# Kernel tuning notes

Hardware: AMD Instinct MI355X
Metric: run time of the kernel (lower is better)

## Reference

```python
import jax, jax.numpy as jnp
import numpy as np

TIME_UNITS = 10.0
EPS_LN = 1e-5
N_NODES, N_EDGES, BATCH, T_IN = 20000, 320000, 8, 12
H_PROB, H_VEL = 64, 32


def _layernorm(x, g, b):
    mu = jnp.mean(x, axis=-1, keepdims=True)
    var = jnp.mean((x - mu) ** 2, axis=-1, keepdims=True)
    return (x - mu) / jnp.sqrt(var + EPS_LN) * g + b


def setup_inputs() -> dict:
    key = jax.random.key(0)
    ks = jax.random.split(key, 20)
    s = 0.1
    inp = {}
    inp['upstream'] = jax.random.uniform(ks[0], (N_EDGES, BATCH, T_IN), jnp.float32)
    inp['downstream'] = jax.random.uniform(ks[1], (N_EDGES, BATCH, T_IN), jnp.float32)
    inp['feature'] = jax.random.uniform(ks[2], (N_NODES, BATCH, T_IN), jnp.float32)
    inp['distance'] = jax.random.uniform(ks[3], (N_EDGES,), jnp.float32, 10.0, 500.0)
    inp['src'] = jax.random.randint(ks[4], (N_EDGES,), 0, N_NODES, jnp.int32)
    inp['dst'] = jax.random.randint(ks[5], (N_EDGES,), 0, N_NODES, jnp.int32)
    inp['fc_w'] = jax.random.normal(ks[6], (H_PROB, T_IN), jnp.float32) * s
    inp['attn_w'] = jax.random.normal(ks[7], (1, 2 * H_PROB + 1), jnp.float32) * s
    inp['ln2_g'] = jnp.ones((2 * H_PROB + 1,), jnp.float32)
    inp['ln2_b'] = jnp.zeros((2 * H_PROB + 1,), jnp.float32)
    inp['v11_w'] = jax.random.normal(ks[8], (H_VEL, T_IN), jnp.float32) * s
    inp['v11_b'] = jnp.zeros((H_VEL,), jnp.float32)
    inp['ln11_g'] = jnp.ones((H_VEL,), jnp.float32)
    inp['ln11_b'] = jnp.zeros((H_VEL,), jnp.float32)
    inp['v12_w'] = jax.random.normal(ks[9], (1, H_VEL), jnp.float32) * s
    inp['v12_b'] = jnp.zeros((1,), jnp.float32)
    inp['v21_w'] = jax.random.normal(ks[10], (H_VEL, T_IN), jnp.float32) * s
    inp['v21_b'] = jnp.zeros((H_VEL,), jnp.float32)
    inp['ln21_g'] = jnp.ones((H_VEL,), jnp.float32)
    inp['ln21_b'] = jnp.zeros((H_VEL,), jnp.float32)
    inp['v22_w'] = jax.random.normal(ks[11], (1, H_VEL), jnp.float32) * s
    inp['v22_b'] = jnp.zeros((1,), jnp.float32)
    inp['v3_w'] = jax.random.normal(ks[12], (1, 2), jnp.float32) * s
    inp['v3_b'] = jnp.zeros((1,), jnp.float32)
    inp['alpha'] = jnp.ones((N_EDGES, 1), jnp.float32)
    return inp


def reference(upstream, downstream, feature, distance, src, dst,
              fc_w, attn_w, ln2_g, ln2_b,
              v11_w, v11_b, ln11_g, ln11_b, v12_w, v12_b,
              v21_w, v21_b, ln21_g, ln21_b, v22_w, v22_b,
              v3_w, v3_b, alpha):
    N, B, T = feature.shape
    Tf = jnp.asarray(T, feature.dtype)

    # --- Velocity_Model_NAM (eval mode: dropout = identity) ---
    def branch(x, w1, b1, g, bn, w2, b2):
        h = jax.nn.relu(_layernorm(x @ w1.T + b1, g, bn))
        return jax.nn.sigmoid(h @ w2.T + b2)  # [E,B,1]

    xu = branch(upstream, v11_w, v11_b, ln11_g, ln11_b, v12_w, v12_b)
    xd = branch(downstream, v21_w, v21_b, ln21_g, ln21_b, v22_w, v22_b)
    v = jnp.log1p(jnp.exp((jnp.concatenate([xu, xd], -1) @ v3_w.T + v3_b)[..., 0]))  # [E,B]

    # --- per-edge travel time and diffusion kernel ---
    Tt = distance[:, None] / (v + 1e-5)                # [E,B]
    T_idx = jnp.round(Tt / TIME_UNITS)
    T_idx = jnp.where(T_idx < 0, 0.0, T_idx)
    T_idx = jnp.where(T_idx > Tf, Tf - 1.0, T_idx)     # strictly > T_in, as in masked_fill
    F = 1.0 / (1.0 + alpha * Tt)                       # [E,B]
    n = jnp.maximum(Tf - T_idx, 1.0)                   # sequence length per (edge,batch)
    t = jnp.arange(T, dtype=feature.dtype)
    mask = t < n[..., None]
    expo = jnp.maximum(n[..., None] - 1.0 - t, 0.0)    # decreasing exponents n-1..0
    diffusion = jnp.where(mask, F[..., None] * jnp.power(1.0 - F[..., None], expo), 0.0)  # [E,B,T]

    # --- Probabilistic_Model: embeddings + edge softmax normalized per SOURCE node ---
    z = feature @ fc_w.T                               # [N,B,64]
    zc = jnp.concatenate([z[src], z[dst], jax.lax.stop_gradient(v)[..., None]], -1)  # [E,B,129]
    a = jax.nn.leaky_relu((_layernorm(zc, ln2_g, ln2_b) @ attn_w.T)[..., 0], 0.01)   # [E,B]
    m = jax.ops.segment_max(a, src, num_segments=N)
    ex = jnp.exp(a - m[src])
    den = jax.ops.segment_sum(ex, src, num_segments=N)
    score = ex / den[src]

    # --- mailbox reduce: attention-weighted diffusion prediction per destination ---
    pred_edge = jnp.sum(diffusion * feature[src], -1)  # [E,B]
    pred = jax.ops.segment_sum(score * pred_edge, dst, num_segments=N)  # [N,B]
    return pred
```

## Files before the change

kernel.cpp:

```cpp
#include <hip/hip_runtime.h>
#include <math.h>

#define TB 8
#define TT 12
#define HV 32

typedef float v2f __attribute__((ext_vector_type(2)));

__device__ __forceinline__ float vel_branch32(const v2f xv[6],
    const float* __restrict__ w1, const float* __restrict__ b1,
    const float* __restrict__ g,  const float* __restrict__ bn,
    const float* __restrict__ w2, float b2) {
  v2f h2[HV/2];
  v2f s1v = {0.f, 0.f}, s2v = {0.f, 0.f};
#pragma unroll
  for (int jp = 0; jp < HV/2; ++jp) {
    const float* w0 = w1 + (2*jp)   * TT;
    const float* w1r = w1 + (2*jp+1) * TT;
    v2f p0 = {0.f, 0.f}, p1 = {0.f, 0.f};
#pragma unroll
    for (int k = 0; k < 6; ++k) {
      p0 = __builtin_elementwise_fma(xv[k], *(const v2f*)(w0  + 2*k), p0);
      p1 = __builtin_elementwise_fma(xv[k], *(const v2f*)(w1r + 2*k), p1);
    }
    v2f bj = *(const v2f*)(b1 + 2*jp);
    v2f hv = {p0.x + p0.y + bj.x, p1.x + p1.y + bj.y};
    h2[jp] = hv;
    s1v += hv;
    s2v = __builtin_elementwise_fma(hv, hv, s2v);
  }
  float s1 = s1v.x + s1v.y;
  float s2 = s2v.x + s2v.y;
  float mu  = s1 * (1.f/HV);
  float var = s2 * (1.f/HV) - mu*mu;
  float inv = 1.f / sqrtf(var + 1e-5f);
  v2f mu2  = {mu, mu};
  v2f inv2 = {inv, inv};
  v2f zero = {0.f, 0.f};
  v2f acc2 = {b2, 0.f};
#pragma unroll
  for (int jp = 0; jp < HV/2; ++jp) {
    v2f gv  = *(const v2f*)(g  + 2*jp);
    v2f bnv = *(const v2f*)(bn + 2*jp);
    v2f w2v = *(const v2f*)(w2 + 2*jp);
    v2f yl = __builtin_elementwise_fma((h2[jp] - mu2) * inv2, gv, bnv);
    yl = __builtin_elementwise_max(yl, zero);
    acc2 = __builtin_elementwise_fma(yl, w2v, acc2);
  }
  float acc = acc2.x + acc2.y;
  return 1.f / (1.f + __expf(-acc));
}

__device__ __noinline__ double vel_branch64(const float* x,
    const float* __restrict__ w1, const float* __restrict__ b1,
    const float* __restrict__ g,  const float* __restrict__ bn,
    const float* __restrict__ w2, float b2) {
  double s1 = 0.0, s2 = 0.0;
  for (int j = 0; j < HV; ++j) {
    double hj = (double)b1[j];
    for (int t = 0; t < TT; ++t) hj = fma((double)x[t], (double)w1[j*TT+t], hj);
    s1 += hj;
    s2 = fma(hj, hj, s2);
  }
  double mu  = s1 / (double)HV;
  double var = s2 / (double)HV - mu*mu;
  double inv = 1.0 / sqrt(var + 1e-5);
  double acc = (double)b2;
  for (int j = 0; j < HV; ++j) {
    double hj = (double)b1[j];
    for (int t = 0; t < TT; ++t) hj = fma((double)x[t], (double)w1[j*TT+t], hj);
    double yl = (hj - mu) * inv * (double)g[j] + (double)bn[j];
    if (yl < 0.0) yl = 0.0;
    acc = fma(yl, (double)w2[j], acc);
  }
  return 1.0 / (1.0 + exp(-acc));
}

__global__ void __launch_bounds__(256) k_zero_prep(
    float* __restrict__ den, float* __restrict__ pred, int nb,
    const float* __restrict__ attn_w, const float* __restrict__ ln2_g,
    const float* __restrict__ ln2_b, float* __restrict__ scal) {
  int idx = blockIdx.x * blockDim.x + threadIdx.x;
  for (int i = idx; i < nb; i += gridDim.x * blockDim.x) { den[i] = 0.f; pred[i] = 0.f; }
  if (blockIdx.x == 0) {
    __shared__ float sg[256], sb[256];
    float a = 0.f, b = 0.f;
    if (threadIdx.x < 129) {
      float w = attn_w[threadIdx.x];
      a = w * ln2_g[threadIdx.x];
      b = w * ln2_b[threadIdx.x];
    }
    sg[threadIdx.x] = a; sb[threadIdx.x] = b;
    __syncthreads();
    for (int s = 128; s > 0; s >>= 1) {
      if (threadIdx.x < s) { sg[threadIdx.x] += sg[threadIdx.x+s]; sb[threadIdx.x] += sb[threadIdx.x+s]; }
      __syncthreads();
    }
    if (threadIdx.x == 0) { scal[0] = sg[0]; scal[1] = sb[0]; }
  }
}

__global__ void __launch_bounds__(256, 2) k_node(
    const float* __restrict__ feature, const float* __restrict__ fc_w,
    const float* __restrict__ attn_w,  const float* __restrict__ ln2_g,
    float4* __restrict__ nodepre, int n_nodes) {
  int idx = blockIdx.x * blockDim.x + threadIdx.x;
  int total = n_nodes * TB;
  if (idx >= total) return;
  const float4* f4 = (const float4*)(feature + (size_t)idx * TT);
  float4 fa = f4[0], fb = f4[1], fcv = f4[2];
  v2f xv[6] = {{fa.x,fa.y},{fa.z,fa.w},{fb.x,fb.y},{fb.z,fb.w},{fcv.x,fcv.y},{fcv.z,fcv.w}};
  float q = 0.f, r = 0.f, ps = 0.f, pd = 0.f;
#pragma unroll 8
  for (int i = 0; i < 64; ++i) {
    v2f p = {0.f, 0.f};
#pragma unroll
    for (int k = 0; k < 6; ++k)
      p = __builtin_elementwise_fma(xv[k], *(const v2f*)(fc_w + i*TT + 2*k), p);
    float z = p.x + p.y;
    q += z;
    r  = fmaf(z, z, r);
    ps = fmaf(z, attn_w[i]      * ln2_g[i],      ps);
    pd = fmaf(z, attn_w[64 + i] * ln2_g[64 + i], pd);
  }
  nodepre[idx] = make_float4(q, r, ps, pd);
}

__global__ void __launch_bounds__(256, 2) k_edge1(
    const float* __restrict__ upstream, const float* __restrict__ downstream,
    const float* __restrict__ feature,  const float* __restrict__ distance,
    const int* __restrict__ src, const int* __restrict__ dst,
    const float* __restrict__ attn_w, const float* __restrict__ ln2_g,
    const float* __restrict__ v11_w, const float* __restrict__ v11_b,
    const float* __restrict__ ln11_g, const float* __restrict__ ln11_b,
    const float* __restrict__ v12_w, const float* __restrict__ v12_b,
    const float* __restrict__ v21_w, const float* __restrict__ v21_b,
    const float* __restrict__ ln21_g, const float* __restrict__ ln21_b,
    const float* __restrict__ v22_w, const float* __restrict__ v22_b,
    const float* __restrict__ v3_w, const float* __restrict__ v3_b,
    const float* __restrict__ alpha,
    const float4* __restrict__ nodepre, const float* __restrict__ scal,
    float2* __restrict__ epbuf, float* __restrict__ den,
    int n_edges) {
  int idx = blockIdx.x * blockDim.x + threadIdx.x;
  if (idx >= n_edges * TB) return;
  int e = idx >> 3, b = idx & 7;

  int s = src[e], d = dst[e];
  float dist = distance[e];
  float al   = alpha[e];
  const float4* f4 = (const float4*)(feature + ((size_t)s * TB + b) * TT);
  float4 f0 = f4[0], f1 = f4[1], f2 = f4[2];
  float4 nps = nodepre[(size_t)s * TB + b];
  float4 npd = nodepre[(size_t)d * TB + b];

  float xu, xd;
  {
    const float4* u4 = (const float4*)(upstream + (size_t)idx * TT);
    float4 a0 = u4[0], a1 = u4[1], a2 = u4[2];
    v2f xv[6] = {{a0.x,a0.y},{a0.z,a0.w},{a1.x,a1.y},{a1.z,a1.w},{a2.x,a2.y},{a2.z,a2.w}};
    xu = vel_branch32(xv, v11_w, v11_b, ln11_g, ln11_b, v12_w, v12_b[0]);
  }
  {
    const float4* d4 = (const float4*)(downstream + (size_t)idx * TT);
    float4 c0 = d4[0], c1 = d4[1], c2 = d4[2];
    v2f xv[6] = {{c0.x,c0.y},{c0.z,c0.w},{c1.x,c1.y},{c1.z,c1.w},{c2.x,c2.y},{c2.z,c2.w}};
    xd = vel_branch32(xv, v21_w, v21_b, ln21_g, ln21_b, v22_w, v22_b[0]);
  }
  float y = fmaf(xu, v3_w[0], fmaf(xd, v3_w[1], v3_b[0]));
  float v = fmaxf(y, 0.f) + __logf(1.f + __expf(-fabsf(y)));

  float tt  = dist / (v + 1e-5f);
  float th  = tt * 0.1f;
  float tif = rintf(th);

  if (fabsf(th - tif) < 1e-3f && tt < 120.0f) {
    const float* xr_u = upstream   + (size_t)idx * TT;
    const float* xr_d = downstream + (size_t)idx * TT;
    double xu64 = vel_branch64(xr_u, v11_w, v11_b, ln11_g, ln11_b, v12_w, v12_b[0]);
    double xd64 = vel_branch64(xr_d, v21_w, v21_b, ln21_g, ln21_b, v22_w, v22_b[0]);
    double y64  = xu64*(double)v3_w[0] + xd64*(double)v3_w[1] + (double)v3_b[0];
    double v64  = log1p(exp(y64));
    double tt64 = (double)dist / (v64 + 1e-5);
    v   = (float)v64;
    tt  = (float)tt64;
    tif = (float)rint(tt64 * 0.1);
  }

  int ti = (int)tif;
  ti = ti < 0 ? 0 : (ti > TT ? TT - 1 : ti);
  int n = TT - ti; n = n < 1 ? 1 : n;

  float F  = 1.f / fmaf(al, tt, 1.f);
  float om = 1.f - F;

  float feat[TT] = {f0.x,f0.y,f0.z,f0.w, f1.x,f1.y,f1.z,f1.w, f2.x,f2.y,f2.z,f2.w};
  float acc = 0.f;
#pragma unroll
  for (int t = 0; t < TT; ++t) {
    acc = (t < n) ? fmaf(acc, om, feat[t]) : acc;
  }
  float pe = F * acc;

  float sum   = nps.x + npd.x + v;
  float sumsq = nps.y + npd.y + v*v;
  float mu  = sum * (1.f/129.f);
  float var = sumsq * (1.f/129.f) - mu*mu;
  float S1  = nps.z + npd.w + v * attn_w[128] * ln2_g[128];
  float aa  = (S1 - mu*scal[0]) / sqrtf(var + 1e-5f) + scal[1];
  float a   = aa >= 0.f ? aa : 0.01f*aa;
  float ex  = __expf(a);

  epbuf[idx] = make_float2(ex, pe);
  atomicAdd(&den[s * TB + b], ex);
}

__global__ void __launch_bounds__(256) k_edge2(
    const int* __restrict__ src, const int* __restrict__ dst,
    const float2* __restrict__ epbuf,
    const float* __restrict__ den, float* __restrict__ pred, int n_edges) {
  int idx = blockIdx.x * blockDim.x + threadIdx.x;
  if (idx >= n_edges * TB) return;
  int e = idx >> 3, b = idx & 7;
  float2 ep = epbuf[idx];
  float score = ep.x / den[src[e] * TB + b];
  atomicAdd(&pred[dst[e] * TB + b], score * ep.y);
}

extern "C" void kernel_launch(void* const* d_in, const int* in_sizes, int n_in,
                              void* d_out, int out_size, void* d_ws, size_t ws_size,
                              hipStream_t stream) {
  const float* upstream   = (const float*)d_in[0];
  const float* downstream = (const float*)d_in[1];
  const float* feature    = (const float*)d_in[2];
  const float* distance   = (const float*)d_in[3];
  const int*   src        = (const int*)d_in[4];
  const int*   dst        = (const int*)d_in[5];
  const float* fc_w   = (const float*)d_in[6];
  const float* attn_w = (const float*)d_in[7];
  const float* ln2_g  = (const float*)d_in[8];
  const float* ln2_b  = (const float*)d_in[9];
  const float* v11_w  = (const float*)d_in[10];
  const float* v11_b  = (const float*)d_in[11];
  const float* ln11_g = (const float*)d_in[12];
  const float* ln11_b = (const float*)d_in[13];
  const float* v12_w  = (const float*)d_in[14];
  const float* v12_b  = (const float*)d_in[15];
  const float* v21_w  = (const float*)d_in[16];
  const float* v21_b  = (const float*)d_in[17];
  const float* ln21_g = (const float*)d_in[18];
  const float* ln21_b = (const float*)d_in[19];
  const float* v22_w  = (const float*)d_in[20];
  const float* v22_b  = (const float*)d_in[21];
  const float* v3_w   = (const float*)d_in[22];
  const float* v3_b   = (const float*)d_in[23];
  const float* alpha  = (const float*)d_in[24];

  int E  = in_sizes[4];
  int N  = in_sizes[2] / (TB * TT);
  int NB = N * TB;
  int EB = E * TB;

  float*  ws      = (float*)d_ws;
  float4* nodepre = (float4*)ws;
  float2* epbuf   = (float2*)(ws + 4 * (size_t)NB);
  float*  den     = ws + 4 * (size_t)NB + 2 * (size_t)EB;
  float*  scal    = den + NB;
  float*  pred    = (float*)d_out;

  int blk = 256;
  k_zero_prep<<<(NB + blk - 1) / blk, blk, 0, stream>>>(den, pred, NB, attn_w, ln2_g, ln2_b, scal);
  k_node<<<(NB + blk - 1) / blk, blk, 0, stream>>>(feature, fc_w, attn_w, ln2_g, nodepre, N);
  k_edge1<<<(EB + blk - 1) / blk, blk, 0, stream>>>(
      upstream, downstream, feature, distance, src, dst,
      attn_w, ln2_g,
      v11_w, v11_b, ln11_g, ln11_b, v12_w, v12_b,
      v21_w, v21_b, ln21_g, ln21_b, v22_w, v22_b,
      v3_w, v3_b, alpha,
      nodepre, scal, epbuf, den, E);
  k_edge2<<<(EB + blk - 1) / blk, blk, 0, stream>>>(src, dst, epbuf, den, pred, E);
}
```

Baseline: 187.6 us.

## Fold velocity-MLP layernorm into precomputed weights and process four rows per thread

A new k_fold kernel precomputes mean-centred, gain-scaled first-layer weights and a quadratic-form matrix, so the per-row layernorm variance comes from x^T M x with no separate hidden-mean pass. k_edge1 now handles four batch rows per thread, sharing the edge metadata loads and reusing each loaded weight across four rows. It also writes epbuf with float4 stores and raises the occupancy hint in launch bounds. This trades register pressure and some float rounding behaviour (the variance now comes from a different formula) for fewer FLOPs and fewer loads.

```diff
diff --git a/kernel.cpp b/kernel.cpp
--- a/kernel.cpp
+++ b/kernel.cpp
@@ -6,50 +6,6 @@
 #define HV 32
 
 typedef float v2f __attribute__((ext_vector_type(2)));
-
-__device__ __forceinline__ float vel_branch32(const v2f xv[6],
-    const float* __restrict__ w1, const float* __restrict__ b1,
-    const float* __restrict__ g,  const float* __restrict__ bn,
-    const float* __restrict__ w2, float b2) {
-  v2f h2[HV/2];
-  v2f s1v = {0.f, 0.f}, s2v = {0.f, 0.f};
-#pragma unroll
-  for (int jp = 0; jp < HV/2; ++jp) {
-    const float* w0 = w1 + (2*jp)   * TT;
-    const float* w1r = w1 + (2*jp+1) * TT;
-    v2f p0 = {0.f, 0.f}, p1 = {0.f, 0.f};
-#pragma unroll
-    for (int k = 0; k < 6; ++k) {
-      p0 = __builtin_elementwise_fma(xv[k], *(const v2f*)(w0  + 2*k), p0);
-      p1 = __builtin_elementwise_fma(xv[k], *(const v2f*)(w1r + 2*k), p1);
-    }
-    v2f bj = *(const v2f*)(b1 + 2*jp);
-    v2f hv = {p0.x + p0.y + bj.x, p1.x + p1.y + bj.y};
-    h2[jp] = hv;
-    s1v += hv;
-    s2v = __builtin_elementwise_fma(hv, hv, s2v);
-  }
-  float s1 = s1v.x + s1v.y;
-  float s2 = s2v.x + s2v.y;
-  float mu  = s1 * (1.f/HV);
-  float var = s2 * (1.f/HV) - mu*mu;
-  float inv = 1.f / sqrtf(var + 1e-5f);
-  v2f mu2  = {mu, mu};
-  v2f inv2 = {inv, inv};
-  v2f zero = {0.f, 0.f};
-  v2f acc2 = {b2, 0.f};
-#pragma unroll
-  for (int jp = 0; jp < HV/2; ++jp) {
-    v2f gv  = *(const v2f*)(g  + 2*jp);
-    v2f bnv = *(const v2f*)(bn + 2*jp);
-    v2f w2v = *(const v2f*)(w2 + 2*jp);
-    v2f yl = __builtin_elementwise_fma((h2[jp] - mu2) * inv2, gv, bnv);
-    yl = __builtin_elementwise_max(yl, zero);
-    acc2 = __builtin_elementwise_fma(yl, w2v, acc2);
-  }
-  float acc = acc2.x + acc2.y;
-  return 1.f / (1.f + __expf(-acc));
-}
 
 __device__ __noinline__ double vel_branch64(const float* x,
     const float* __restrict__ w1, const float* __restrict__ b1,
@@ -74,6 +30,59 @@
     acc = fma(yl, (double)w2[j], acc);
   }
   return 1.0 / (1.0 + exp(-acc));
+}
+
+__global__ void __launch_bounds__(256) k_fold(
+    const float* __restrict__ v11_w, const float* __restrict__ v11_b,
+    const float* __restrict__ ln11_g, const float* __restrict__ ln11_b,
+    const float* __restrict__ v12_w,
+    const float* __restrict__ v21_w, const float* __restrict__ v21_b,
+    const float* __restrict__ ln21_g, const float* __restrict__ ln21_b,
+    const float* __restrict__ v22_w,
+    float* __restrict__ fold) {
+  int br = blockIdx.x;
+  const float* W1 = br ? v21_w : v11_w;
+  const float* B1 = br ? v21_b : v11_b;
+  const float* G  = br ? ln21_g : ln11_g;
+  const float* BN = br ? ln21_b : ln11_b;
+  const float* W2 = br ? v22_w : v12_w;
+  float* stream = fold + br * 672;
+  float* Mblk   = stream + 512;
+  int tid = threadIdx.x;
+  float wbar[TT];
+  for (int t = 0; t < TT; ++t) {
+    float sw = 0.f;
+    for (int j = 0; j < HV; ++j) sw += W1[j*TT + t];
+    wbar[t] = sw * (1.f/HV);
+  }
+  float bbar = 0.f;
+  for (int j = 0; j < HV; ++j) bbar += B1[j];
+  bbar *= (1.f/HV);
+
+  if (tid < HV) {
+    int j = tid;
+    float gj = G[j];
+    for (int t = 0; t < TT; ++t) stream[j*16 + t] = gj * (W1[j*TT + t] - wbar[t]);
+    stream[j*16 + 12] = gj * (B1[j] - bbar);
+    stream[j*16 + 13] = BN[j];
+    stream[j*16 + 14] = W2[j];
+    stream[j*16 + 15] = 0.f;
+  } else if (tid < 32 + 144) {
+    int p = tid - 32, t = p / TT, s = p % TT;
+    float m = 0.f;
+    for (int j = 0; j < HV; ++j)
+      m += (W1[j*TT + t] - wbar[t]) * (W1[j*TT + s] - wbar[s]);
+    Mblk[p] = m * (1.f/HV);
+  } else if (tid < 176 + 12) {
+    int t = tid - 176;
+    float rr = 0.f;
+    for (int j = 0; j < HV; ++j) rr += (B1[j] - bbar) * (W1[j*TT + t] - wbar[t]);
+    Mblk[144 + t] = rr * (2.f/HV);
+  } else if (tid == 188) {
+    float kk = 0.f;
+    for (int j = 0; j < HV; ++j) { float c = B1[j] - bbar; kk += c*c; }
+    Mblk[156] = kk * (1.f/HV);
+  }
 }
 
 __global__ void __launch_bounds__(256) k_zero_prep(
@@ -126,7 +135,7 @@
   nodepre[idx] = make_float4(q, r, ps, pd);
 }
 
-__global__ void __launch_bounds__(256, 2) k_edge1(
+__global__ void __launch_bounds__(256, 3) k_edge1(
     const float* __restrict__ upstream, const float* __restrict__ downstream,
     const float* __restrict__ feature,  const float* __restrict__ distance,
     const int* __restrict__ src, const int* __restrict__ dst,
@@ -139,80 +148,174 @@
     const float* __restrict__ v22_w, const float* __restrict__ v22_b,
     const float* __restrict__ v3_w, const float* __restrict__ v3_b,
     const float* __restrict__ alpha,
+    const float* __restrict__ fold,
     const float4* __restrict__ nodepre, const float* __restrict__ scal,
     float2* __restrict__ epbuf, float* __restrict__ den,
-    int n_edges) {
+    int n_quads) {
   int idx = blockIdx.x * blockDim.x + threadIdx.x;
-  if (idx >= n_edges * TB) return;
-  int e = idx >> 3, b = idx & 7;
+  if (idx >= n_quads) return;
+  int e    = idx >> 1;
+  int b0   = (idx & 1) * 4;
+  int row0 = idx * 4;
 
   int s = src[e], d = dst[e];
   float dist = distance[e];
   float al   = alpha[e];
-  const float4* f4 = (const float4*)(feature + ((size_t)s * TB + b) * TT);
-  float4 f0 = f4[0], f1 = f4[1], f2 = f4[2];
-  float4 nps = nodepre[(size_t)s * TB + b];
-  float4 npd = nodepre[(size_t)d * TB + b];
-
-  float xu, xd;
+  float w3a = v3_w[0], w3b = v3_w[1];
+
+  float ys[4];
+  { float b3 = v3_b[0]; ys[0]=b3; ys[1]=b3; ys[2]=b3; ys[3]=b3; }
+
+#pragma unroll 1
+  for (int br = 0; br < 2; ++br) {
+    const float* rows = br ? downstream : upstream;
+    const float* st   = fold + br * 672;
+    const float* Mb   = st + 512;
+    float b2  = br ? v22_b[0] : v12_b[0];
+    float w3v = br ? w3b : w3a;
+
+    v2f xv[4][6];
+    {
+      const float4* r4 = (const float4*)(rows + (size_t)row0 * TT);
+#pragma unroll
+      for (int r = 0; r < 4; ++r) {
+        float4 q0 = r4[r*3+0], q1 = r4[r*3+1], q2 = r4[r*3+2];
+        xv[r][0] = (v2f){q0.x,q0.y}; xv[r][1] = (v2f){q0.z,q0.w};
+        xv[r][2] = (v2f){q1.x,q1.y}; xv[r][3] = (v2f){q1.z,q1.w};
+        xv[r][4] = (v2f){q2.x,q2.y}; xv[r][5] = (v2f){q2.z,q2.w};
+      }
+    }
+
+    v2f y[4][6];
+#pragma unroll
+    for (int k = 0; k < 6; ++k) {
+      v2f rv = *(const v2f*)(Mb + 144 + 2*k);
+      y[0][k]=rv; y[1][k]=rv; y[2][k]=rv; y[3][k]=rv;
+    }
+#pragma unroll
+    for (int t = 0; t < TT; ++t) {
+      const float* mrow = Mb + t*TT;
+#pragma unroll
+      for (int k = 0; k < 6; ++k) {
+        v2f mv = *(const v2f*)(mrow + 2*k);
+#pragma unroll
+        for (int r = 0; r < 4; ++r) {
+          float xs = xv[r][t>>1][t&1];
+          v2f xb = {xs, xs};
+          y[r][k] = __builtin_elementwise_fma(xb, mv, y[r][k]);
+        }
+      }
+    }
+    float kc = Mb[156];
+    float sig[4], iv[4], acc[4];
+#pragma unroll
+    for (int r = 0; r < 4; ++r) {
+      v2f q = xv[r][0] * y[r][0];
+#pragma unroll
+      for (int k = 1; k < 6; ++k) q = __builtin_elementwise_fma(xv[r][k], y[r][k], q);
+      float varp = q.x + q.y + kc + 1e-5f;
+      float is = 1.f / sqrtf(varp);
+      iv[r] = is; sig[r] = varp * is; acc[r] = 0.f;
+    }
+
+#pragma unroll
+    for (int j = 0; j < HV; ++j) {
+      const float* sj = st + j*16;
+      v2f a0 = *(const v2f*)(sj+0),  a1 = *(const v2f*)(sj+2),  a2 = *(const v2f*)(sj+4);
+      v2f a3 = *(const v2f*)(sj+6),  a4 = *(const v2f*)(sj+8),  a5 = *(const v2f*)(sj+10);
+      float Cj = sj[12], bnj = sj[13], wj2 = sj[14];
+#pragma unroll
+      for (int r = 0; r < 4; ++r) {
+        v2f p = xv[r][0] * a0;
+        p = __builtin_elementwise_fma(xv[r][1], a1, p);
+        p = __builtin_elementwise_fma(xv[r][2], a2, p);
+        p = __builtin_elementwise_fma(xv[r][3], a3, p);
+        p = __builtin_elementwise_fma(xv[r][4], a4, p);
+        p = __builtin_elementwise_fma(xv[r][5], a5, p);
+        float u = p.x + p.y + Cj;
+        float z = fmaf(sig[r], bnj, u);
+        z = fmaxf(z, 0.f);
+        acc[r] = fmaf(z, wj2, acc[r]);
+      }
+    }
+#pragma unroll
+    for (int r = 0; r < 4; ++r) {
+      float val = fmaf(acc[r], iv[r], b2);
+      float sg = 1.f / (1.f + __expf(-val));
+      ys[r] = fmaf(sg, w3v, ys[r]);
+    }
+  }
+
+  float4 F[12];
   {
-    const float4* u4 = (const float4*)(upstream + (size_t)idx * TT);
-    float4 a0 = u4[0], a1 = u4[1], a2 = u4[2];
-    v2f xv[6] = {{a0.x,a0.y},{a0.z,a0.w},{a1.x,a1.y},{a1.z,a1.w},{a2.x,a2.y},{a2.z,a2.w}};
-    xu = vel_branch32(xv, v11_w, v11_b, ln11_g, ln11_b, v12_w, v12_b[0]);
-  }
-  {
-    const float4* d4 = (const float4*)(downstream + (size_t)idx * TT);
-    float4 c0 = d4[0], c1 = d4[1], c2 = d4[2];
-    v2f xv[6] = {{c0.x,c0.y},{c0.z,c0.w},{c1.x,c1.y},{c1.z,c1.w},{c2.x,c2.y},{c2.z,c2.w}};
-    xd = vel_branch32(xv, v21_w, v21_b, ln21_g, ln21_b, v22_w, v22_b[0]);
-  }
-  float y = fmaf(xu, v3_w[0], fmaf(xd, v3_w[1], v3_b[0]));
-  float v = fmaxf(y, 0.f) + __logf(1.f + __expf(-fabsf(y)));
-
-  float tt  = dist / (v + 1e-5f);
-  float th  = tt * 0.1f;
-  float tif = rintf(th);
-
-  if (fabsf(th - tif) < 1e-3f && tt < 120.0f) {
-    const float* xr_u = upstream   + (size_t)idx * TT;
-    const float* xr_d = downstream + (size_t)idx * TT;
-    double xu64 = vel_branch64(xr_u, v11_w, v11_b, ln11_g, ln11_b, v12_w, v12_b[0]);
-    double xd64 = vel_branch64(xr_d, v21_w, v21_b, ln21_g, ln21_b, v22_w, v22_b[0]);
-    double y64  = xu64*(double)v3_w[0] + xd64*(double)v3_w[1] + (double)v3_b[0];
-    double v64  = log1p(exp(y64));
-    double tt64 = (double)dist / (v64 + 1e-5);
-    v   = (float)v64;
-    tt  = (float)tt64;
-    tif = (float)rint(tt64 * 0.1);
-  }
-
-  int ti = (int)tif;
-  ti = ti < 0 ? 0 : (ti > TT ? TT - 1 : ti);
-  int n = TT - ti; n = n < 1 ? 1 : n;
-
-  float F  = 1.f / fmaf(al, tt, 1.f);
-  float om = 1.f - F;
-
-  float feat[TT] = {f0.x,f0.y,f0.z,f0.w, f1.x,f1.y,f1.z,f1.w, f2.x,f2.y,f2.z,f2.w};
-  float acc = 0.f;
-#pragma unroll
-  for (int t = 0; t < TT; ++t) {
-    acc = (t < n) ? fmaf(acc, om, feat[t]) : acc;
-  }
-  float pe = F * acc;
-
-  float sum   = nps.x + npd.x + v;
-  float sumsq = nps.y + npd.y + v*v;
-  float mu  = sum * (1.f/129.f);
-  float var = sumsq * (1.f/129.f) - mu*mu;
-  float S1  = nps.z + npd.w + v * attn_w[128] * ln2_g[128];
-  float aa  = (S1 - mu*scal[0]) / sqrtf(var + 1e-5f) + scal[1];
-  float a   = aa >= 0.f ? aa : 0.01f*aa;
-  float ex  = __expf(a);
-
-  epbuf[idx] = make_float2(ex, pe);
-  atomicAdd(&den[s * TB + b], ex);
+    const float4* f4 = (const float4*)(feature + ((size_t)s * TB + b0) * TT);
+#pragma unroll
+    for (int i = 0; i < 12; ++i) F[i] = f4[i];
+  }
+  float4 np_s[4], np_d[4];
+#pragma unroll
+  for (int r = 0; r < 4; ++r) {
+    np_s[r] = nodepre[(size_t)s * TB + b0 + r];
+    np_d[r] = nodepre[(size_t)d * TB + b0 + r];
+  }
+  float aw128 = attn_w[128] * ln2_g[128];
+  float sc0 = scal[0], sc1 = scal[1];
+
+  float exv[4], pev[4];
+#pragma unroll
+  for (int r = 0; r < 4; ++r) {
+    float yv = ys[r];
+    float v = fmaxf(yv, 0.f) + __logf(1.f + __expf(-fabsf(yv)));
+    float tt  = dist / (v + 1e-5f);
+    float th  = tt * 0.1f;
+    float tif = rintf(th);
+
+    if (fabsf(th - tif) < 1e-3f && tt < 120.0f) {
+      const float* xr_u = upstream   + (size_t)(row0 + r) * TT;
+      const float* xr_d = downstream + (size_t)(row0 + r) * TT;
+      double xu64 = vel_branch64(xr_u, v11_w, v11_b, ln11_g, ln11_b, v12_w, v12_b[0]);
+      double xd64 = vel_branch64(xr_d, v21_w, v21_b, ln21_g, ln21_b, v22_w, v22_b[0]);
+      double y64  = xu64*(double)w3a + xd64*(double)w3b + (double)v3_b[0];
+      double v64  = log1p(exp(y64));
+      double tt64 = (double)dist / (v64 + 1e-5);
+      v   = (float)v64;
+      tt  = (float)tt64;
+      tif = (float)rint(tt64 * 0.1);
+    }
+
+    int ti = (int)tif;
+    ti = ti < 0 ? 0 : (ti > TT ? TT - 1 : ti);
+    int n = TT - ti; n = n < 1 ? 1 : n;
+
+    float Fk = 1.f / fmaf(al, tt, 1.f);
+    float om = 1.f - Fk;
+
+    float4 g0 = F[r*3], g1 = F[r*3+1], g2 = F[r*3+2];
+    float feat[TT] = {g0.x,g0.y,g0.z,g0.w, g1.x,g1.y,g1.z,g1.w, g2.x,g2.y,g2.z,g2.w};
+    float accf = 0.f;
+#pragma unroll
+    for (int t = 0; t < TT; ++t) {
+      accf = (t < n) ? fmaf(accf, om, feat[t]) : accf;
+    }
+    float pe = Fk * accf;
+
+    float4 nps = np_s[r], npd = np_d[r];
+    float sum   = nps.x + npd.x + v;
+    float sumsq = nps.y + npd.y + v*v;
+    float mu  = sum * (1.f/129.f);
+    float var = sumsq * (1.f/129.f) - mu*mu;
+    float S1  = nps.z + npd.w + v * aw128;
+    float aa  = (S1 - mu*sc0) / sqrtf(var + 1e-5f) + sc1;
+    float a   = aa >= 0.f ? aa : 0.01f*aa;
+    exv[r] = __expf(a);
+    pev[r] = pe;
+    atomicAdd(&den[s * TB + b0 + r], exv[r]);
+  }
+
+  float4 e0 = make_float4(exv[0], pev[0], exv[1], pev[1]);
+  float4 e1 = make_float4(exv[2], pev[2], exv[3], pev[3]);
+  ((float4*)epbuf)[idx*2]     = e0;
+  ((float4*)epbuf)[idx*2 + 1] = e1;
 }
 
 __global__ void __launch_bounds__(256) k_edge2(
@@ -260,23 +363,27 @@
   int N  = in_sizes[2] / (TB * TT);
   int NB = N * TB;
   int EB = E * TB;
+  int NQ = EB / 4;
 
   float*  ws      = (float*)d_ws;
-  float4* nodepre = (float4*)ws;
-  float2* epbuf   = (float2*)(ws + 4 * (size_t)NB);
-  float*  den     = ws + 4 * (size_t)NB + 2 * (size_t)EB;
+  float*  foldbuf = ws;
+  float4* nodepre = (float4*)(ws + 1344);
+  float2* epbuf   = (float2*)(ws + 1344 + 4 * (size_t)NB);
+  float*  den     = ws + 1344 + 4 * (size_t)NB + 2 * (size_t)EB;
   float*  scal    = den + NB;
   float*  pred    = (float*)d_out;
 
   int blk = 256;
+  k_fold<<<2, blk, 0, stream>>>(v11_w, v11_b, ln11_g, ln11_b, v12_w,
+                                v21_w, v21_b, ln21_g, ln21_b, v22_w, foldbuf);
   k_zero_prep<<<(NB + blk - 1) / blk, blk, 0, stream>>>(den, pred, NB, attn_w, ln2_g, ln2_b, scal);
   k_node<<<(NB + blk - 1) / blk, blk, 0, stream>>>(feature, fc_w, attn_w, ln2_g, nodepre, N);
-  k_edge1<<<(EB + blk - 1) / blk, blk, 0, stream>>>(
+  k_edge1<<<(NQ + blk - 1) / blk, blk, 0, stream>>>(
       upstream, downstream, feature, distance, src, dst,
       attn_w, ln2_g,
       v11_w, v11_b, ln11_g, ln11_b, v12_w, v12_b,
       v21_w, v21_b, ln21_g, ln21_b, v22_w, v22_b,
       v3_w, v3_b, alpha,
-      nodepre, scal, epbuf, den, E);
+      foldbuf, nodepre, scal, epbuf, den, NQ);
   k_edge2<<<(EB + blk - 1) / blk, blk, 0, stream>>>(src, dst, epbuf, den, pred, E);
 }
```

After: 281.0 us. 1.5x slower.

## Defer fp64 rounding-edge recompute to a separate fix kernel, stage weights in LDS

Applied to the files above, without the earlier changes.

Takes the rare double-precision recompute of near-integer travel times out of the main edge kernel. The main kernel appends flagged edge indices to a worklist with an atomic counter, and a small follow-up kernel recomputes those edges and corrects den by the difference in exp values. The velocity MLP weights are packed into one buffer by a new fold kernel and loaded into shared memory per block, so the main kernel no longer carries a divergent fp64 path that raises register pressure. The cost is two extra launches, a block-wide LDS load and sync in every block, and a worklist capped at a quarter of the edges.

```diff
diff --git a/kernel.cpp b/kernel.cpp
--- a/kernel.cpp
+++ b/kernel.cpp
@@ -7,15 +7,23 @@
 
 typedef float v2f __attribute__((ext_vector_type(2)));
 
-__device__ __forceinline__ float vel_branch32(const v2f xv[6],
-    const float* __restrict__ w1, const float* __restrict__ b1,
-    const float* __restrict__ g,  const float* __restrict__ bn,
-    const float* __restrict__ w2, float b2) {
+#define PK_W1 0
+#define PK_B1 384
+#define PK_G  416
+#define PK_BN 448
+#define PK_W2 480
+
+__device__ __forceinline__ float vel_branch32(const v2f xv[6], const float* swb, float b2) {
+  const float* w1 = swb + PK_W1;
+  const float* b1 = swb + PK_B1;
+  const float* g  = swb + PK_G;
+  const float* bn = swb + PK_BN;
+  const float* w2 = swb + PK_W2;
   v2f h2[HV/2];
   v2f s1v = {0.f, 0.f}, s2v = {0.f, 0.f};
 #pragma unroll
   for (int jp = 0; jp < HV/2; ++jp) {
-    const float* w0 = w1 + (2*jp)   * TT;
+    const float* w0  = w1 + (2*jp)   * TT;
     const float* w1r = w1 + (2*jp+1) * TT;
     v2f p0 = {0.f, 0.f}, p1 = {0.f, 0.f};
 #pragma unroll
@@ -51,7 +59,7 @@
   return 1.f / (1.f + __expf(-acc));
 }
 
-__device__ __noinline__ double vel_branch64(const float* x,
+__device__ double vel_branch64(const float* x,
     const float* __restrict__ w1, const float* __restrict__ b1,
     const float* __restrict__ g,  const float* __restrict__ bn,
     const float* __restrict__ w2, float b2) {
@@ -76,13 +84,41 @@
   return 1.0 / (1.0 + exp(-acc));
 }
 
+__global__ void __launch_bounds__(256) k_fold(
+    const float* __restrict__ v11_w, const float* __restrict__ v11_b,
+    const float* __restrict__ ln11_g, const float* __restrict__ ln11_b,
+    const float* __restrict__ v12_w,
+    const float* __restrict__ v21_w, const float* __restrict__ v21_b,
+    const float* __restrict__ ln21_g, const float* __restrict__ ln21_b,
+    const float* __restrict__ v22_w,
+    float* __restrict__ pack) {
+  int br = blockIdx.x;
+  const float* W1 = br ? v21_w : v11_w;
+  const float* B1 = br ? v21_b : v11_b;
+  const float* G  = br ? ln21_g : ln11_g;
+  const float* BN = br ? ln21_b : ln11_b;
+  const float* W2 = br ? v22_w : v12_w;
+  float* p = pack + br * 512;
+  for (int i = threadIdx.x; i < 512; i += blockDim.x) {
+    float val;
+    if (i < PK_B1)      val = W1[i];
+    else if (i < PK_G)  val = B1[i - PK_B1];
+    else if (i < PK_BN) val = G[i - PK_G];
+    else if (i < PK_W2) val = BN[i - PK_BN];
+    else                val = W2[i - PK_W2];
+    p[i] = val;
+  }
+}
+
 __global__ void __launch_bounds__(256) k_zero_prep(
     float* __restrict__ den, float* __restrict__ pred, int nb,
     const float* __restrict__ attn_w, const float* __restrict__ ln2_g,
-    const float* __restrict__ ln2_b, float* __restrict__ scal) {
+    const float* __restrict__ ln2_b, float* __restrict__ scal,
+    int* __restrict__ fixcnt) {
   int idx = blockIdx.x * blockDim.x + threadIdx.x;
   for (int i = idx; i < nb; i += gridDim.x * blockDim.x) { den[i] = 0.f; pred[i] = 0.f; }
   if (blockIdx.x == 0) {
+    if (threadIdx.x == 0) fixcnt[0] = 0;
     __shared__ float sg[256], sb[256];
     float a = 0.f, b = 0.f;
     if (threadIdx.x < 129) {
@@ -131,6 +167,88 @@
     const float* __restrict__ feature,  const float* __restrict__ distance,
     const int* __restrict__ src, const int* __restrict__ dst,
     const float* __restrict__ attn_w, const float* __restrict__ ln2_g,
+    const float* __restrict__ v12_b, const float* __restrict__ v22_b,
+    const float* __restrict__ v3_w, const float* __restrict__ v3_b,
+    const float* __restrict__ alpha,
+    const float* __restrict__ pack,
+    const float4* __restrict__ nodepre, const float* __restrict__ scal,
+    float2* __restrict__ epbuf, float* __restrict__ den,
+    int* __restrict__ fixcnt, int* __restrict__ fixlist, int fixcap,
+    int n_edges) {
+  __shared__ float sw[1024];
+  ((float4*)sw)[threadIdx.x] = ((const float4*)pack)[threadIdx.x];
+  __syncthreads();
+
+  int idx = blockIdx.x * blockDim.x + threadIdx.x;
+  if (idx >= n_edges * TB) return;
+  int e = idx >> 3, b = idx & 7;
+
+  int s = src[e], d = dst[e];
+  float dist = distance[e];
+  float al   = alpha[e];
+  const float4* f4 = (const float4*)(feature + ((size_t)s * TB + b) * TT);
+  float4 f0 = f4[0], f1 = f4[1], f2 = f4[2];
+  float4 nps = nodepre[(size_t)s * TB + b];
+  float4 npd = nodepre[(size_t)d * TB + b];
+
+  float xu, xd;
+  {
+    const float4* u4 = (const float4*)(upstream + (size_t)idx * TT);
+    float4 a0 = u4[0], a1 = u4[1], a2 = u4[2];
+    v2f xv[6] = {{a0.x,a0.y},{a0.z,a0.w},{a1.x,a1.y},{a1.z,a1.w},{a2.x,a2.y},{a2.z,a2.w}};
+    xu = vel_branch32(xv, sw, v12_b[0]);
+  }
+  {
+    const float4* d4 = (const float4*)(downstream + (size_t)idx * TT);
+    float4 c0 = d4[0], c1 = d4[1], c2 = d4[2];
+    v2f xv[6] = {{c0.x,c0.y},{c0.z,c0.w},{c1.x,c1.y},{c1.z,c1.w},{c2.x,c2.y},{c2.z,c2.w}};
+    xd = vel_branch32(xv, sw + 512, v22_b[0]);
+  }
+  float y = fmaf(xu, v3_w[0], fmaf(xd, v3_w[1], v3_b[0]));
+  float v = fmaxf(y, 0.f) + __logf(1.f + __expf(-fabsf(y)));
+
+  float tt  = dist / (v + 1e-5f);
+  float th  = tt * 0.1f;
+  float tif = rintf(th);
+
+  if (fabsf(th - tif) < 1e-3f && tt < 120.0f) {
+    int p = atomicAdd(fixcnt, 1);
+    if (p < fixcap) fixlist[p] = idx;
+  }
+
+  int ti = (int)tif;
+  ti = ti < 0 ? 0 : (ti > TT ? TT - 1 : ti);
+  int n = TT - ti; n = n < 1 ? 1 : n;
+
+  float F  = 1.f / fmaf(al, tt, 1.f);
+  float om = 1.f - F;
+
+  float feat[TT] = {f0.x,f0.y,f0.z,f0.w, f1.x,f1.y,f1.z,f1.w, f2.x,f2.y,f2.z,f2.w};
+  float acc = 0.f;
+#pragma unroll
+  for (int t = 0; t < TT; ++t) {
+    acc = (t < n) ? fmaf(acc, om, feat[t]) : acc;
+  }
+  float pe = F * acc;
+
+  float sum   = nps.x + npd.x + v;
+  float sumsq = nps.y + npd.y + v*v;
+  float mu  = sum * (1.f/129.f);
+  float var = sumsq * (1.f/129.f) - mu*mu;
+  float S1  = nps.z + npd.w + v * attn_w[128] * ln2_g[128];
+  float aa  = (S1 - mu*scal[0]) / sqrtf(var + 1e-5f) + scal[1];
+  float a   = aa >= 0.f ? aa : 0.01f*aa;
+  float ex  = __expf(a);
+
+  epbuf[idx] = make_float2(ex, pe);
+  atomicAdd(&den[s * TB + b], ex);
+}
+
+__global__ void __launch_bounds__(256) k_fix(
+    const float* __restrict__ upstream, const float* __restrict__ downstream,
+    const float* __restrict__ feature,  const float* __restrict__ distance,
+    const int* __restrict__ src, const int* __restrict__ dst,
+    const float* __restrict__ attn_w, const float* __restrict__ ln2_g,
     const float* __restrict__ v11_w, const float* __restrict__ v11_b,
     const float* __restrict__ ln11_g, const float* __restrict__ ln11_b,
     const float* __restrict__ v12_w, const float* __restrict__ v12_b,
@@ -141,40 +259,17 @@
     const float* __restrict__ alpha,
     const float4* __restrict__ nodepre, const float* __restrict__ scal,
     float2* __restrict__ epbuf, float* __restrict__ den,
-    int n_edges) {
-  int idx = blockIdx.x * blockDim.x + threadIdx.x;
-  if (idx >= n_edges * TB) return;
-  int e = idx >> 3, b = idx & 7;
-
-  int s = src[e], d = dst[e];
-  float dist = distance[e];
-  float al   = alpha[e];
-  const float4* f4 = (const float4*)(feature + ((size_t)s * TB + b) * TT);
-  float4 f0 = f4[0], f1 = f4[1], f2 = f4[2];
-  float4 nps = nodepre[(size_t)s * TB + b];
-  float4 npd = nodepre[(size_t)d * TB + b];
-
-  float xu, xd;
-  {
-    const float4* u4 = (const float4*)(upstream + (size_t)idx * TT);
-    float4 a0 = u4[0], a1 = u4[1], a2 = u4[2];
-    v2f xv[6] = {{a0.x,a0.y},{a0.z,a0.w},{a1.x,a1.y},{a1.z,a1.w},{a2.x,a2.y},{a2.z,a2.w}};
-    xu = vel_branch32(xv, v11_w, v11_b, ln11_g, ln11_b, v12_w, v12_b[0]);
-  }
-  {
-    const float4* d4 = (const float4*)(downstream + (size_t)idx * TT);
-    float4 c0 = d4[0], c1 = d4[1], c2 = d4[2];
-    v2f xv[6] = {{c0.x,c0.y},{c0.z,c0.w},{c1.x,c1.y},{c1.z,c1.w},{c2.x,c2.y},{c2.z,c2.w}};
-    xd = vel_branch32(xv, v21_w, v21_b, ln21_g, ln21_b, v22_w, v22_b[0]);
-  }
-  float y = fmaf(xu, v3_w[0], fmaf(xd, v3_w[1], v3_b[0]));
-  float v = fmaxf(y, 0.f) + __logf(1.f + __expf(-fabsf(y)));
-
-  float tt  = dist / (v + 1e-5f);
-  float th  = tt * 0.1f;
-  float tif = rintf(th);
-
-  if (fabsf(th - tif) < 1e-3f && tt < 120.0f) {
+    const int* __restrict__ fixcnt, const int* __restrict__ fixlist, int fixcap) {
+  int cnt = fixcnt[0];
+  if (cnt > fixcap) cnt = fixcap;
+  int stride = gridDim.x * blockDim.x;
+  for (int i = blockIdx.x * blockDim.x + threadIdx.x; i < cnt; i += stride) {
+    int idx = fixlist[i];
+    int e = idx >> 3, b = idx & 7;
+    int s = src[e], d = dst[e];
+    float dist = distance[e];
+    float al   = alpha[e];
+
     const float* xr_u = upstream   + (size_t)idx * TT;
     const float* xr_d = downstream + (size_t)idx * TT;
     double xu64 = vel_branch64(xr_u, v11_w, v11_b, ln11_g, ln11_b, v12_w, v12_b[0]);
@@ -182,37 +277,37 @@
     double y64  = xu64*(double)v3_w[0] + xd64*(double)v3_w[1] + (double)v3_b[0];
     double v64  = log1p(exp(y64));
     double tt64 = (double)dist / (v64 + 1e-5);
-    v   = (float)v64;
-    tt  = (float)tt64;
-    tif = (float)rint(tt64 * 0.1);
-  }
-
-  int ti = (int)tif;
-  ti = ti < 0 ? 0 : (ti > TT ? TT - 1 : ti);
-  int n = TT - ti; n = n < 1 ? 1 : n;
-
-  float F  = 1.f / fmaf(al, tt, 1.f);
-  float om = 1.f - F;
-
-  float feat[TT] = {f0.x,f0.y,f0.z,f0.w, f1.x,f1.y,f1.z,f1.w, f2.x,f2.y,f2.z,f2.w};
-  float acc = 0.f;
-#pragma unroll
-  for (int t = 0; t < TT; ++t) {
-    acc = (t < n) ? fmaf(acc, om, feat[t]) : acc;
-  }
-  float pe = F * acc;
-
-  float sum   = nps.x + npd.x + v;
-  float sumsq = nps.y + npd.y + v*v;
-  float mu  = sum * (1.f/129.f);
-  float var = sumsq * (1.f/129.f) - mu*mu;
-  float S1  = nps.z + npd.w + v * attn_w[128] * ln2_g[128];
-  float aa  = (S1 - mu*scal[0]) / sqrtf(var + 1e-5f) + scal[1];
-  float a   = aa >= 0.f ? aa : 0.01f*aa;
-  float ex  = __expf(a);
-
-  epbuf[idx] = make_float2(ex, pe);
-  atomicAdd(&den[s * TB + b], ex);
+    float v   = (float)v64;
+    float tt  = (float)tt64;
+    float tif = (float)rint(tt64 * 0.1);
+
+    int ti = (int)tif;
+    ti = ti < 0 ? 0 : (ti > TT ? TT - 1 : ti);
+    int n = TT - ti; n = n < 1 ? 1 : n;
+
+    float F  = 1.f / fmaf(al, tt, 1.f);
+    float om = 1.f - F;
+
+    const float* feat = feature + ((size_t)s * TB + b) * TT;
+    float acc = 0.f;
+    for (int t = 0; t < n; ++t) acc = fmaf(acc, om, feat[t]);
+    float pe = F * acc;
+
+    float4 nps = nodepre[(size_t)s * TB + b];
+    float4 npd = nodepre[(size_t)d * TB + b];
+    float sum   = nps.x + npd.x + v;
+    float sumsq = nps.y + npd.y + v*v;
+    float mu  = sum * (1.f/129.f);
+    float var = sumsq * (1.f/129.f) - mu*mu;
+    float S1  = nps.z + npd.w + v * attn_w[128] * ln2_g[128];
+    float aa  = (S1 - mu*scal[0]) / sqrtf(var + 1e-5f) + scal[1];
+    float a   = aa >= 0.f ? aa : 0.01f*aa;
+    float ex  = __expf(a);
+
+    float2 old = epbuf[idx];
+    epbuf[idx] = make_float2(ex, pe);
+    atomicAdd(&den[s * TB + b], ex - old.x);
+  }
 }
 
 __global__ void __launch_bounds__(256) k_edge2(
@@ -260,23 +355,33 @@
   int N  = in_sizes[2] / (TB * TT);
   int NB = N * TB;
   int EB = E * TB;
+  int fixcap = EB / 4;
 
   float*  ws      = (float*)d_ws;
   float4* nodepre = (float4*)ws;
   float2* epbuf   = (float2*)(ws + 4 * (size_t)NB);
   float*  den     = ws + 4 * (size_t)NB + 2 * (size_t)EB;
   float*  scal    = den + NB;
+  float*  pack    = scal + 2;
+  int*    fixcnt  = (int*)(pack + 1024);
+  int*    fixlist = fixcnt + 4;
   float*  pred    = (float*)d_out;
 
   int blk = 256;
-  k_zero_prep<<<(NB + blk - 1) / blk, blk, 0, stream>>>(den, pred, NB, attn_w, ln2_g, ln2_b, scal);
+  k_fold<<<2, blk, 0, stream>>>(v11_w, v11_b, ln11_g, ln11_b, v12_w,
+                                v21_w, v21_b, ln21_g, ln21_b, v22_w, pack);
+  k_zero_prep<<<(NB + blk - 1) / blk, blk, 0, stream>>>(den, pred, NB, attn_w, ln2_g, ln2_b, scal, fixcnt);
   k_node<<<(NB + blk - 1) / blk, blk, 0, stream>>>(feature, fc_w, attn_w, ln2_g, nodepre, N);
   k_edge1<<<(EB + blk - 1) / blk, blk, 0, stream>>>(
+      upstream, downstream, feature, distance, src, dst,
+      attn_w, ln2_g, v12_b, v22_b, v3_w, v3_b, alpha,
+      pack, nodepre, scal, epbuf, den, fixcnt, fixlist, fixcap, E);
+  k_fix<<<64, blk, 0, stream>>>(
       upstream, downstream, feature, distance, src, dst,
       attn_w, ln2_g,
       v11_w, v11_b, ln11_g, ln11_b, v12_w, v12_b,
       v21_w, v21_b, ln21_g, ln21_b, v22_w, v22_b,
       v3_w, v3_b, alpha,
-      nodepre, scal, epbuf, den, E);
+      nodepre, scal, epbuf, den, fixcnt, fixlist, fixcap);
   k_edge2<<<(EB + blk - 1) / blk, blk, 0, stream>>>(src, dst, epbuf, den, pred, E);
 }
```

New measurement: 199.5 us. 6.3% more time.
